# Optimization experiments

Hardware: AMD Instinct MI355X
Metric: run time of the kernel (lower is better)

Reference implementation:

```python
import jax, jax.numpy as jnp
import numpy as np

NUM_GROUPS = 32
EPS = 1e-6


def setup_inputs() -> dict:
    key = jax.random.key(0)
    ks = jax.random.split(key, 4)
    B, C, H, W = 16, 512, 32, 32
    x = jax.random.normal(ks[0], (B, C, H, W), dtype=jnp.float32)
    norm_w = jnp.ones((C,), dtype=jnp.float32)
    norm_b = jnp.zeros((C,), dtype=jnp.float32)
    qkv_w = jax.random.normal(ks[1], (3 * C, C), dtype=jnp.float32) * (1.0 / np.sqrt(C))
    qkv_b = jnp.zeros((3 * C,), dtype=jnp.float32)
    proj_w = jax.random.normal(ks[2], (C, C), dtype=jnp.float32) * (1.0 / np.sqrt(C))
    proj_b = jnp.zeros((C,), dtype=jnp.float32)
    return {"x": x, "norm_w": norm_w, "norm_b": norm_b, "qkv_w": qkv_w,
            "qkv_b": qkv_b, "proj_w": proj_w, "proj_b": proj_b}


def _group_norm(x, w, b):
    B, C, H, W = x.shape
    g = NUM_GROUPS
    xg = x.reshape(B, g, C // g, H * W)
    mu = xg.mean(axis=(2, 3), keepdims=True)
    var = xg.var(axis=(2, 3), keepdims=True)
    xn = (xg - mu) * jax.lax.rsqrt(var + EPS)
    xn = xn.reshape(B, C, H, W)
    return xn * w[None, :, None, None] + b[None, :, None, None]


def reference(x, norm_w, norm_b, qkv_w, qkv_b, proj_w, proj_b):
    B, C, H, W = x.shape
    h = _group_norm(x, norm_w, norm_b)
    # 1x1 conv == channel GEMM
    qkv = jnp.einsum('oc,bchw->bohw', qkv_w, h) + qkv_b[None, :, None, None]
    q, k, v = jnp.split(qkv, 3, axis=1)
    N = H * W
    q = q.reshape(B, C, N)  # (b, c, n)
    k = k.reshape(B, C, N)
    v = v.reshape(B, C, N)
    scale = jnp.asarray(C, x.dtype) ** -0.5
    attn = jnp.einsum('bci,bcj->bij', q, k) * scale  # (b, Nq, Nk)
    attn = jax.nn.softmax(attn, axis=2)
    o = jnp.einsum('bcj,bij->bci', v, attn).reshape(B, C, H, W)
    out = jnp.einsum('oc,bchw->bohw', proj_w, o) + proj_b[None, :, None, None]
    return x + out
```

## Files before the change

kernel.cpp:

```cpp
#include <hip/hip_runtime.h>

typedef unsigned short u16;
typedef __bf16 bf16x8 __attribute__((ext_vector_type(8)));
typedef float f32x4 __attribute__((ext_vector_type(4)));

#define AS1 __attribute__((address_space(1)))
#define AS3 __attribute__((address_space(3)))


__device__ __forceinline__ u16 f2bf(float f) {
  union { float f; unsigned u; } v; v.f = f;
  return (u16)((v.u + 0x7fffu + ((v.u >> 16) & 1u)) >> 16);
}

__device__ __forceinline__ f32x4 mfma16(bf16x8 a, bf16x8 b, f32x4 c) {
  return __builtin_amdgcn_mfma_f32_16x16x32_bf16(a, b, c, 0, 0, 0);
}

__device__ __forceinline__ void stage_tile(const u16* __restrict__ src, size_t ld,
                                           u16* lds, int wv, int lane) {
#pragma unroll
  for (int h2 = 0; h2 < 2; h2++) {
    int rbase = wv * 32 + h2 * 16;
    int row = rbase + (lane >> 2);
    int segd = (lane & 3) ^ ((row >> 1) & 3);
    __builtin_amdgcn_global_load_lds(
        (const AS1 void*)(src + (size_t)row * ld + segd * 8),
        (AS3 void*)(lds + rbase * 32), 16, 0, 0);
  }
}

__device__ __forceinline__ bf16x8 ldsfrag(const u16* lds, int row, int rowq) {
  int q = rowq ^ ((row >> 1) & 3);
  return *(const bf16x8*)(lds + row * 32 + q * 8);
}

template<int NT>
__device__ __forceinline__ void gemm_core(const u16* __restrict__ A, int lda,
                                          const u16* __restrict__ B, int ldb,
                                          u16* lds, f32x4 (&acc)[4][4],
                                          int wave, int lane) {
  u16* sA0 = lds;        u16* sA1 = lds + 4096;
  u16* sB0 = lds + 8192; u16* sB1 = lds + 12288;
  int wm = wave >> 1, wn = wave & 1;
  int col = lane & 15, rq = lane >> 4;
#pragma unroll
  for (int m = 0; m < 4; m++)
#pragma unroll
    for (int n = 0; n < 4; n++) acc[m][n] = (f32x4){0.f, 0.f, 0.f, 0.f};

  stage_tile(A, lda, sA0, wave, lane);
  stage_tile(B, ldb, sB0, wave, lane);
  stage_tile(A + 32, lda, sA1, wave, lane);
  stage_tile(B + 32, ldb, sB1, wave, lane);

  for (int t = 0; t < NT; t++) {
    u16* cA = (t & 1) ? sA1 : sA0;
    u16* cB = (t & 1) ? sB1 : sB0;
    if (t < NT - 1) {
      asm volatile("s_waitcnt vmcnt(4)" ::: "memory");
    } else {
      asm volatile("s_waitcnt vmcnt(0)" ::: "memory");
    }
    __builtin_amdgcn_sched_barrier(0);
    __builtin_amdgcn_s_barrier();
    __builtin_amdgcn_sched_barrier(0);
    bf16x8 af[4], bfr[4];
#pragma unroll
    for (int n = 0; n < 4; n++) bfr[n] = ldsfrag(cB, wn * 64 + n * 16 + col, rq);
#pragma unroll
    for (int m = 0; m < 4; m++) af[m] = ldsfrag(cA, wm * 64 + m * 16 + col, rq);
#pragma unroll
    for (int m = 0; m < 4; m++)
#pragma unroll
      for (int n = 0; n < 4; n++) acc[m][n] = mfma16(af[m], bfr[n], acc[m][n]);
    __builtin_amdgcn_sched_barrier(0);
    __builtin_amdgcn_s_barrier();
    if (t + 2 < NT) {
      stage_tile(A + (size_t)(t + 2) * 32, lda, cA, wave, lane);
      stage_tile(B + (size_t)(t + 2) * 32, ldb, cB, wave, lane);
    }
  }
}

__global__ __launch_bounds__(256) void gn_fused(const float* __restrict__ x,
                                                const float* __restrict__ gw,
                                                const float* __restrict__ gb,
                                                u16* __restrict__ h) {
  __shared__ float buf[16 * 1032];
  __shared__ float ls[4], lss[4];
  int bg = blockIdx.x;
  int b = bg >> 5, g = bg & 31;
  const float4* p = (const float4*)(x + (size_t)bg * 16384);
  float s = 0.f, ss = 0.f;
  for (int i = threadIdx.x; i < 4096; i += 256) {
    float4 v = p[i];
    int c = i >> 8, n = (i & 255) * 4;
    *(float4*)&buf[c * 1032 + n] = v;
    s  += v.x + v.y + v.z + v.w;
    ss += v.x*v.x + v.y*v.y + v.z*v.z + v.w*v.w;
  }
  for (int d = 32; d; d >>= 1) { s += __shfl_down(s, d); ss += __shfl_down(ss, d); }
  int wv = threadIdx.x >> 6;
  if ((threadIdx.x & 63) == 0) { ls[wv] = s; lss[wv] = ss; }
  __syncthreads();
  float m = (ls[0] + ls[1] + ls[2] + ls[3]) * (1.f / 16384.f);
  float var = (lss[0] + lss[1] + lss[2] + lss[3]) * (1.f / 16384.f) - m * m;
  float r = rsqrtf(var + 1e-6f);
  int c0 = g * 16;
  float w[16], bb[16];
#pragma unroll
  for (int c = 0; c < 16; c++) {
    w[c] = gw[c0 + c] * r;
    bb[c] = gb[c0 + c] - m * w[c];
  }
  for (int n = threadIdx.x; n < 1024; n += 256) {
    u16 o[16];
#pragma unroll
    for (int c = 0; c < 16; c++) o[c] = f2bf(buf[c * 1032 + n] * w[c] + bb[c]);
    u16* dst = h + (((size_t)((b << 10) | n)) << 9) + c0;
    *(uint4*)dst = *(uint4*)o;
    *(uint4*)(dst + 8) = *(uint4*)(o + 8);
  }
}

__global__ __launch_bounds__(256) void cast_bf16(const float* __restrict__ src,
                                                 u16* __restrict__ dst, int n) {
  int i = (blockIdx.x * 256 + threadIdx.x) * 4;
  if (i < n) {
    float4 v = *(const float4*)(src + i);
    dst[i] = f2bf(v.x); dst[i+1] = f2bf(v.y); dst[i+2] = f2bf(v.z); dst[i+3] = f2bf(v.w);
  }
}

__global__ __launch_bounds__(256, 4) void gemm_qkv(const u16* __restrict__ A,
                                                   const u16* __restrict__ Bn,
                                                   const float* __restrict__ bias,
                                                   u16* __restrict__ q_nc,
                                                   u16* __restrict__ k_nc,
                                                   u16* __restrict__ v) {
  __shared__ u16 lds[16384];
  int bid = blockIdx.x;
  int xcd = bid & 7, r = bid >> 3;
  int mb = r % 12, nb = xcd * 16 + r / 12;
  int m0 = mb * 128, n0 = nb * 128;
  int t = threadIdx.x, wave = t >> 6, lane = t & 63;
  int wm = wave >> 1, wn = wave & 1;
  int col = lane & 15, rq = lane >> 4;
  f32x4 acc[4][4];
  gemm_core<16>(A + (size_t)m0 * 512, 512, Bn + (size_t)n0 * 512, 512,
                lds, acc, wave, lane);
  if (mb < 8) {
    u16* dst = (mb < 4) ? q_nc : k_nc;
#pragma unroll
    for (int i = 0; i < 4; i++)
#pragma unroll
      for (int j = 0; j < 4; j++) {
        int o = m0 + wm * 64 + i * 16 + rq * 4;
        int bn = n0 + wn * 64 + j * 16 + col;
        u16 tmp[4];
#pragma unroll
        for (int rr = 0; rr < 4; rr++) tmp[rr] = f2bf(acc[i][j][rr] + bias[o + rr]);
        *(uint2*)(dst + (size_t)bn * 512 + (o & 511)) = *(uint2*)tmp;
      }
  } else {
#pragma unroll
    for (int i = 0; i < 4; i++)
#pragma unroll
      for (int j = 0; j < 4; j++)
#pragma unroll
        for (int rr = 0; rr < 4; rr++) {
          int o = m0 + wm * 64 + i * 16 + rq * 4 + rr;
          int bn = n0 + wn * 64 + j * 16 + col;
          v[(size_t)(o & 511) * 16384 + bn] = f2bf(acc[i][j][rr] + bias[o]);
        }
  }
}

__global__ __launch_bounds__(256, 4) void gemm_s(const u16* __restrict__ q_nc,
                                                 const u16* __restrict__ k_nc,
                                                 u16* __restrict__ E,
                                                 float* __restrict__ part) {
  __shared__ u16 lds[16384];
  int bid = blockIdx.x;
  int xcd = bid & 7, r = bid >> 3;
  int b = xcd * 2 + (r & 1);
  int tile = r >> 1;
  int m0 = (tile >> 3) * 128, n0 = (tile & 7) * 128;
  int t = threadIdx.x, wave = t >> 6, lane = t & 63;
  int wm = wave >> 1, wn = wave & 1;
  int col = lane & 15, rq = lane >> 4;
  f32x4 acc[4][4];
  gemm_core<16>(q_nc + ((size_t)(b * 1024 + m0)) * 512, 512,
                k_nc + ((size_t)(b * 1024 + n0)) * 512, 512,
                lds, acc, wave, lane);
  u16* Eb = E + ((size_t)b << 20);
  float* pb = part + ((size_t)b << 14);
  int idx = (n0 >> 6) + wn;
  const float scale = 0.04419417382415922f;
#pragma unroll
  for (int i = 0; i < 4; i++)
#pragma unroll
    for (int rr = 0; rr < 4; rr++) {
      float e[4], rs = 0.f;
#pragma unroll
      for (int j = 0; j < 4; j++) { e[j] = __expf(acc[i][j][rr] * scale); rs += e[j]; }
      rs += __shfl_xor(rs, 1); rs += __shfl_xor(rs, 2);
      rs += __shfl_xor(rs, 4); rs += __shfl_xor(rs, 8);
      int row = m0 + wm * 64 + i * 16 + rq * 4 + rr;
      if (col == 0) pb[row * 16 + idx] = rs;
#pragma unroll
      for (int j = 0; j < 4; j++) {
        int jj = n0 + wn * 64 + j * 16 + col;
        Eb[(size_t)row * 1024 + jj] = f2bf(e[j]);
      }
    }
}

__global__ __launch_bounds__(256) void row_inv2(const float* __restrict__ part,
                                                float* __restrict__ inv) {
  int row = blockIdx.x * 256 + threadIdx.x;
  const float4* p = (const float4*)(part + (size_t)row * 16);
  float4 a = p[0], b = p[1], c = p[2], d = p[3];
  float s = a.x+a.y+a.z+a.w + b.x+b.y+b.z+b.w + c.x+c.y+c.z+c.w + d.x+d.y+d.z+d.w;
  inv[row] = 1.f / s;
}

__global__ __launch_bounds__(256, 4) void gemm_pv(const u16* __restrict__ E,
                                                  const u16* __restrict__ v,
                                                  const float* __restrict__ inv,
                                                  u16* __restrict__ o_nc) {
  __shared__ u16 lds[16384];
  int bid = blockIdx.x;
  int xcd = bid & 7, r = bid >> 3;
  int b = xcd * 2 + (r & 1);
  int tile = r >> 1;
  int m0 = (tile >> 2) * 128, n0 = (tile & 3) * 128;
  int t = threadIdx.x, wave = t >> 6, lane = t & 63;
  int wm = wave >> 1, wn = wave & 1;
  int col = lane & 15, rq = lane >> 4;
  f32x4 acc[4][4];
  gemm_core<32>(E + ((size_t)b << 20) + (size_t)m0 * 1024, 1024,
                v + (size_t)n0 * 16384 + ((size_t)b << 10), 16384,
                lds, acc, wave, lane);
#pragma unroll
  for (int i = 0; i < 4; i++)
#pragma unroll
    for (int rr = 0; rr < 4; rr++) {
      int ii = m0 + wm * 64 + i * 16 + rq * 4 + rr;
      float sc = inv[(b << 10) + ii];
#pragma unroll
      for (int j = 0; j < 4; j++) {
        int cc = n0 + wn * 64 + j * 16 + col;
        o_nc[(((size_t)(b * 1024 + ii)) << 9) + cc] = f2bf(acc[i][j][rr] * sc);
      }
    }
}

__global__ __launch_bounds__(256, 4) void gemm_proj(const u16* __restrict__ A,
                                                    const u16* __restrict__ Bn,
                                                    const float* __restrict__ bias,
                                                    const float* __restrict__ xres,
                                                    float* __restrict__ outp) {
  __shared__ u16 lds[16384];
  int bid = blockIdx.x;
  int xcd = bid & 7, r = bid >> 3;
  int mb = r & 3, nb = xcd * 16 + (r >> 2);
  int m0 = mb * 128, n0 = nb * 128;
  int t = threadIdx.x, wave = t >> 6, lane = t & 63;
  int wm = wave >> 1, wn = wave & 1;
  int col = lane & 15, rq = lane >> 4;
  f32x4 acc[4][4];
  gemm_core<16>(A + (size_t)m0 * 512, 512, Bn + (size_t)n0 * 512, 512,
                lds, acc, wave, lane);
#pragma unroll
  for (int i = 0; i < 4; i++)
#pragma unroll
    for (int j = 0; j < 4; j++)
#pragma unroll
      for (int rr = 0; rr < 4; rr++) {
        int co = m0 + wm * 64 + i * 16 + rq * 4 + rr;
        int bn = n0 + wn * 64 + j * 16 + col;
        int bb = bn >> 10, n = bn & 1023;
        size_t oi = (((size_t)(bb * 512 + co)) << 10) + n;
        outp[oi] = acc[i][j][rr] + bias[co] + xres[oi];
      }
}

extern "C" void kernel_launch(void* const* d_in, const int* in_sizes, int n_in,
                              void* d_out, int out_size, void* d_ws, size_t ws_size,
                              hipStream_t stream) {
  const float* x      = (const float*)d_in[0];
  const float* norm_w = (const float*)d_in[1];
  const float* norm_b = (const float*)d_in[2];
  const float* qkv_w  = (const float*)d_in[3];
  const float* qkv_b  = (const float*)d_in[4];
  const float* proj_w = (const float*)d_in[5];
  const float* proj_b = (const float*)d_in[6];
  float* out = (float*)d_out;

  char* ws = (char*)d_ws;
  size_t off = 0;
  auto alloc = [&](size_t bytes) {
    void* p = ws + off;
    off += (bytes + 255) & ~(size_t)255;
    return p;
  };
  float* part = (float*)alloc((size_t)16384 * 16 * 4);
  float* inv  = (float*)alloc(16384 * 4);
  u16* wq   = (u16*)alloc((size_t)1536 * 512 * 2);
  u16* wp   = (u16*)alloc((size_t)512 * 512 * 2);
  u16* h    = (u16*)alloc((size_t)16384 * 512 * 2);
  u16* q_nc = (u16*)alloc((size_t)16384 * 512 * 2);
  u16* k_nc = (u16*)alloc((size_t)16384 * 512 * 2);
  u16* v    = (u16*)alloc((size_t)512 * 16384 * 2);
  u16* E    = (u16*)alloc((size_t)16 * 1024 * 1024 * 2);
  u16* o_nc = h;
  (void)in_sizes; (void)n_in; (void)out_size; (void)ws_size;

  gn_fused<<<512, 256, 0, stream>>>(x, norm_w, norm_b, h);
  cast_bf16<<<(1536 * 512) / 1024, 256, 0, stream>>>(qkv_w, wq, 1536 * 512);
  cast_bf16<<<(512 * 512) / 1024, 256, 0, stream>>>(proj_w, wp, 512 * 512);
  gemm_qkv<<<1536, 256, 0, stream>>>(wq, h, qkv_b, q_nc, k_nc, v);
  gemm_s<<<1024, 256, 0, stream>>>(q_nc, k_nc, E, part);
  row_inv2<<<64, 256, 0, stream>>>(part, inv);
  gemm_pv<<<512, 256, 0, stream>>>(E, v, inv, o_nc);
  gemm_proj<<<512, 256, 0, stream>>>(wp, o_nc, proj_b, x, out);
}
```

Before: 141.0 us.

## Triple-buffer GEMM LDS pipeline and merge weight cast kernels

The shared GEMM core moves from double to triple buffering. It prefetches three K-tiles ahead, uses graded vmcnt waits and rotates the buffer pointers each iteration. The goal is to hide more global-load latency behind the MFMA work. The cost is 48KB of LDS per block instead of 32KB, and the launch-bounds occupancy hint of 4 is dropped, so fewer blocks may fit per CU. The two weight-cast launches are also merged into one kernel to save a launch.

```diff
diff --git a/kernel.cpp b/kernel.cpp
--- a/kernel.cpp
+++ b/kernel.cpp
@@ -40,8 +40,8 @@
                                           const u16* __restrict__ B, int ldb,
                                           u16* lds, f32x4 (&acc)[4][4],
                                           int wave, int lane) {
-  u16* sA0 = lds;        u16* sA1 = lds + 4096;
-  u16* sB0 = lds + 8192; u16* sB1 = lds + 12288;
+  u16* a0 = lds;         u16* a1 = lds + 4096;  u16* a2 = lds + 8192;
+  u16* b0 = lds + 12288; u16* b1 = lds + 16384; u16* b2 = lds + 20480;
   int wm = wave >> 1, wn = wave & 1;
   int col = lane & 15, rq = lane >> 4;
 #pragma unroll
@@ -49,15 +49,18 @@
 #pragma unroll
     for (int n = 0; n < 4; n++) acc[m][n] = (f32x4){0.f, 0.f, 0.f, 0.f};
 
-  stage_tile(A, lda, sA0, wave, lane);
-  stage_tile(B, ldb, sB0, wave, lane);
-  stage_tile(A + 32, lda, sA1, wave, lane);
-  stage_tile(B + 32, ldb, sB1, wave, lane);
+  stage_tile(A, lda, a0, wave, lane);
+  stage_tile(B, ldb, b0, wave, lane);
+  stage_tile(A + 32, lda, a1, wave, lane);
+  stage_tile(B + 32, ldb, b1, wave, lane);
+  stage_tile(A + 64, lda, a2, wave, lane);
+  stage_tile(B + 64, ldb, b2, wave, lane);
 
   for (int t = 0; t < NT; t++) {
-    u16* cA = (t & 1) ? sA1 : sA0;
-    u16* cB = (t & 1) ? sB1 : sB0;
-    if (t < NT - 1) {
+    int rem = NT - 1 - t;
+    if (rem >= 2) {
+      asm volatile("s_waitcnt vmcnt(8)" ::: "memory");
+    } else if (rem == 1) {
       asm volatile("s_waitcnt vmcnt(4)" ::: "memory");
     } else {
       asm volatile("s_waitcnt vmcnt(0)" ::: "memory");
@@ -67,19 +70,21 @@
     __builtin_amdgcn_sched_barrier(0);
     bf16x8 af[4], bfr[4];
 #pragma unroll
-    for (int n = 0; n < 4; n++) bfr[n] = ldsfrag(cB, wn * 64 + n * 16 + col, rq);
-#pragma unroll
-    for (int m = 0; m < 4; m++) af[m] = ldsfrag(cA, wm * 64 + m * 16 + col, rq);
+    for (int n = 0; n < 4; n++) bfr[n] = ldsfrag(b0, wn * 64 + n * 16 + col, rq);
+#pragma unroll
+    for (int m = 0; m < 4; m++) af[m] = ldsfrag(a0, wm * 64 + m * 16 + col, rq);
 #pragma unroll
     for (int m = 0; m < 4; m++)
 #pragma unroll
       for (int n = 0; n < 4; n++) acc[m][n] = mfma16(af[m], bfr[n], acc[m][n]);
     __builtin_amdgcn_sched_barrier(0);
     __builtin_amdgcn_s_barrier();
-    if (t + 2 < NT) {
-      stage_tile(A + (size_t)(t + 2) * 32, lda, cA, wave, lane);
-      stage_tile(B + (size_t)(t + 2) * 32, ldb, cB, wave, lane);
+    if (t + 3 < NT) {
+      stage_tile(A + (size_t)(t + 3) * 32, lda, a0, wave, lane);
+      stage_tile(B + (size_t)(t + 3) * 32, ldb, b0, wave, lane);
     }
+    u16* ta = a0; a0 = a1; a1 = a2; a2 = ta;
+    u16* tb = b0; b0 = b1; b1 = b2; b2 = tb;
   }
 }
 
@@ -124,22 +129,27 @@
   }
 }
 
-__global__ __launch_bounds__(256) void cast_bf16(const float* __restrict__ src,
-                                                 u16* __restrict__ dst, int n) {
-  int i = (blockIdx.x * 256 + threadIdx.x) * 4;
-  if (i < n) {
-    float4 v = *(const float4*)(src + i);
-    dst[i] = f2bf(v.x); dst[i+1] = f2bf(v.y); dst[i+2] = f2bf(v.z); dst[i+3] = f2bf(v.w);
-  }
-}
-
-__global__ __launch_bounds__(256, 4) void gemm_qkv(const u16* __restrict__ A,
-                                                   const u16* __restrict__ Bn,
-                                                   const float* __restrict__ bias,
-                                                   u16* __restrict__ q_nc,
-                                                   u16* __restrict__ k_nc,
-                                                   u16* __restrict__ v) {
-  __shared__ u16 lds[16384];
+__global__ __launch_bounds__(256) void cast_w(const float* __restrict__ qkv_w,
+                                              float* const ,
+                                              const float* __restrict__ proj_w,
+                                              u16* __restrict__ wq,
+                                              u16* __restrict__ wp) {
+  int bid = blockIdx.x;
+  const float* src = (bid < 768) ? qkv_w : proj_w;
+  u16* dst = (bid < 768) ? wq : wp;
+  int base = (bid < 768) ? bid * 1024 : (bid - 768) * 1024;
+  int i = base + threadIdx.x * 4;
+  float4 v = *(const float4*)(src + i);
+  dst[i] = f2bf(v.x); dst[i+1] = f2bf(v.y); dst[i+2] = f2bf(v.z); dst[i+3] = f2bf(v.w);
+}
+
+__global__ __launch_bounds__(256) void gemm_qkv(const u16* __restrict__ A,
+                                                const u16* __restrict__ Bn,
+                                                const float* __restrict__ bias,
+                                                u16* __restrict__ q_nc,
+                                                u16* __restrict__ k_nc,
+                                                u16* __restrict__ v) {
+  __shared__ u16 lds[24576];
   int bid = blockIdx.x;
   int xcd = bid & 7, r = bid >> 3;
   int mb = r % 12, nb = xcd * 16 + r / 12;
@@ -177,11 +187,11 @@
   }
 }
 
-__global__ __launch_bounds__(256, 4) void gemm_s(const u16* __restrict__ q_nc,
-                                                 const u16* __restrict__ k_nc,
-                                                 u16* __restrict__ E,
-                                                 float* __restrict__ part) {
-  __shared__ u16 lds[16384];
+__global__ __launch_bounds__(256) void gemm_s(const u16* __restrict__ q_nc,
+                                              const u16* __restrict__ k_nc,
+                                              u16* __restrict__ E,
+                                              float* __restrict__ part) {
+  __shared__ u16 lds[24576];
   int bid = blockIdx.x;
   int xcd = bid & 7, r = bid >> 3;
   int b = xcd * 2 + (r & 1);
@@ -226,11 +236,11 @@
   inv[row] = 1.f / s;
 }
 
-__global__ __launch_bounds__(256, 4) void gemm_pv(const u16* __restrict__ E,
-                                                  const u16* __restrict__ v,
-                                                  const float* __restrict__ inv,
-                                                  u16* __restrict__ o_nc) {
-  __shared__ u16 lds[16384];
+__global__ __launch_bounds__(256) void gemm_pv(const u16* __restrict__ E,
+                                               const u16* __restrict__ v,
+                                               const float* __restrict__ inv,
+                                               u16* __restrict__ o_nc) {
+  __shared__ u16 lds[24576];
   int bid = blockIdx.x;
   int xcd = bid & 7, r = bid >> 3;
   int b = xcd * 2 + (r & 1);
@@ -257,12 +267,12 @@
     }
 }
 
-__global__ __launch_bounds__(256, 4) void gemm_proj(const u16* __restrict__ A,
-                                                    const u16* __restrict__ Bn,
-                                                    const float* __restrict__ bias,
-                                                    const float* __restrict__ xres,
-                                                    float* __restrict__ outp) {
-  __shared__ u16 lds[16384];
+__global__ __launch_bounds__(256) void gemm_proj(const u16* __restrict__ A,
+                                                 const u16* __restrict__ Bn,
+                                                 const float* __restrict__ bias,
+                                                 const float* __restrict__ xres,
+                                                 float* __restrict__ outp) {
+  __shared__ u16 lds[24576];
   int bid = blockIdx.x;
   int xcd = bid & 7, r = bid >> 3;
   int mb = r & 3, nb = xcd * 16 + (r >> 2);
@@ -319,8 +329,7 @@
   (void)in_sizes; (void)n_in; (void)out_size; (void)ws_size;
 
   gn_fused<<<512, 256, 0, stream>>>(x, norm_w, norm_b, h);
-  cast_bf16<<<(1536 * 512) / 1024, 256, 0, stream>>>(qkv_w, wq, 1536 * 512);
-  cast_bf16<<<(512 * 512) / 1024, 256, 0, stream>>>(proj_w, wp, 512 * 512);
+  cast_w<<<1024, 256, 0, stream>>>(qkv_w, nullptr, proj_w, wq, wp);
   gemm_qkv<<<1536, 256, 0, stream>>>(wq, h, qkv_b, q_nc, k_nc, v);
   gemm_s<<<1024, 256, 0, stream>>>(q_nc, k_nc, E, part);
   row_inv2<<<64, 256, 0, stream>>>(part, inv);
```

Result: slower. 145.1 us (+2.9%).

## Use 256x256 8-wave GEMM tiles with phased pipeline for QKV and scores

Applied to the files above, without the earlier changes.

Adds a new GEMM core that gives each 512-thread block a 256x256 output tile and a BK=64 double-buffered LDS pipeline. Each K-step is split into four phases, and each phase interleaves the global-to-LDS stage of the next tile with MFMA work under s_setprio. The QKV projection and the QK^T score GEMM now use this core to raise operand reuse and cut global/LDS traffic per FLOP, at the cost of 128KB LDS per block and one block per CU. The two weight-cast launches are merged into one, and the launch-bounds occupancy hints on the PV and projection GEMMs are dropped.

```diff
diff --git a/kernel.cpp b/kernel.cpp
--- a/kernel.cpp
+++ b/kernel.cpp
@@ -36,10 +36,10 @@
 }
 
 template<int NT>
-__device__ __forceinline__ void gemm_core(const u16* __restrict__ A, int lda,
-                                          const u16* __restrict__ B, int ldb,
-                                          u16* lds, f32x4 (&acc)[4][4],
-                                          int wave, int lane) {
+__device__ __forceinline__ void gemm_core2(const u16* __restrict__ A, int lda,
+                                           const u16* __restrict__ B, int ldb,
+                                           u16* lds, f32x4 (&acc)[4][4],
+                                           int wave, int lane) {
   u16* sA0 = lds;        u16* sA1 = lds + 4096;
   u16* sB0 = lds + 8192; u16* sB1 = lds + 12288;
   int wm = wave >> 1, wn = wave & 1;
@@ -80,6 +80,114 @@
       stage_tile(A + (size_t)(t + 2) * 32, lda, cA, wave, lane);
       stage_tile(B + (size_t)(t + 2) * 32, ldb, cB, wave, lane);
     }
+  }
+}
+
+__device__ __forceinline__ void stage_half(const u16* __restrict__ src, size_t ld,
+                                           u16* ldsbase, int wave, int lane) {
+#pragma unroll
+  for (int r = 0; r < 2; r++) {
+    int rb = (r * 8 + wave) * 8;
+    int row = rb + (lane >> 3);
+    int seg = (lane & 7) ^ (row & 7);
+    __builtin_amdgcn_global_load_lds(
+        (const AS1 void*)(src + (size_t)row * ld + seg * 8),
+        (AS3 void*)(ldsbase + rb * 64), 16, 0, 0);
+  }
+}
+
+template<int P>
+__device__ __forceinline__ void phase_read(const u16* cA, const u16* cB,
+                                           bf16x8 (&af)[2][2], bf16x8 (&bfr)[4][2],
+                                           int wm, int wn, int col, int rq) {
+  if constexpr (P == 0) {
+#pragma unroll
+    for (int nf = 0; nf < 4; nf++)
+#pragma unroll
+      for (int kk = 0; kk < 2; kk++) {
+        int row = wn * 64 + nf * 16 + col;
+        bfr[nf][kk] = *(const bf16x8*)(cB + row * 64 + (((kk << 2) + rq) ^ (row & 7)) * 8);
+      }
+  }
+#pragma unroll
+  for (int i = 0; i < 2; i++)
+#pragma unroll
+    for (int kk = 0; kk < 2; kk++) {
+      int row = wm * 128 + (P * 2 + i) * 16 + col;
+      af[i][kk] = *(const bf16x8*)(cA + row * 64 + (((kk << 2) + rq) ^ (row & 7)) * 8);
+    }
+}
+
+template<int P>
+__device__ __forceinline__ void phase_fma(const bf16x8 (&af)[2][2],
+                                          const bf16x8 (&bfr)[4][2],
+                                          f32x4 (&acc)[8][4]) {
+#pragma unroll
+  for (int i = 0; i < 2; i++)
+#pragma unroll
+    for (int kk = 0; kk < 2; kk++)
+#pragma unroll
+      for (int nf = 0; nf < 4; nf++)
+        acc[P * 2 + i][nf] = mfma16(af[i][kk], bfr[nf][kk], acc[P * 2 + i][nf]);
+}
+
+#define RUN_PHASE(P, STAGE_CODE, WAIT_CODE)                                  \
+  {                                                                          \
+    bf16x8 af[2][2];                                                         \
+    phase_read<P>(cA, cB, af, bfr, wm, wn, col, rq);                         \
+    STAGE_CODE;                                                              \
+    WAIT_CODE;                                                               \
+    __builtin_amdgcn_sched_barrier(0);                                       \
+    __builtin_amdgcn_s_barrier();                                            \
+    __builtin_amdgcn_sched_barrier(0);                                       \
+    __builtin_amdgcn_s_setprio(1);                                           \
+    phase_fma<P>(af, bfr, acc);                                              \
+    __builtin_amdgcn_s_setprio(0);                                           \
+    __builtin_amdgcn_sched_barrier(0);                                       \
+    __builtin_amdgcn_s_barrier();                                            \
+    __builtin_amdgcn_sched_barrier(0);                                       \
+  }
+
+template<int NT>
+__device__ __forceinline__ void gemm8_core(const u16* __restrict__ A, int lda,
+                                           const u16* __restrict__ B, int ldb,
+                                           u16* lds, f32x4 (&acc)[8][4],
+                                           int wave, int lane) {
+  u16* Abuf[2] = {lds, lds + 16384};
+  u16* Bbuf[2] = {lds + 32768, lds + 49152};
+  int wm = wave >> 2, wn = wave & 3;
+  int col = lane & 15, rq = lane >> 4;
+#pragma unroll
+  for (int m = 0; m < 8; m++)
+#pragma unroll
+    for (int n = 0; n < 4; n++) acc[m][n] = (f32x4){0.f, 0.f, 0.f, 0.f};
+
+  stage_half(A, lda, Abuf[0], wave, lane);
+  stage_half(A + 128 * (size_t)lda, lda, Abuf[0] + 8192, wave, lane);
+  stage_half(B, ldb, Bbuf[0], wave, lane);
+  stage_half(B + 128 * (size_t)ldb, ldb, Bbuf[0] + 8192, wave, lane);
+  stage_half(B + 64, ldb, Bbuf[1], wave, lane);
+  stage_half(B + 64 + 128 * (size_t)ldb, ldb, Bbuf[1] + 8192, wave, lane);
+  asm volatile("s_waitcnt vmcnt(4)" ::: "memory");
+  __builtin_amdgcn_sched_barrier(0);
+  __builtin_amdgcn_s_barrier();
+  __builtin_amdgcn_sched_barrier(0);
+
+  for (int kt = 0; kt < NT; kt++) {
+    const u16* cA = Abuf[kt & 1];
+    const u16* cB = Bbuf[kt & 1];
+    u16* nA = Abuf[(kt + 1) & 1];
+    u16* nB = Bbuf[kt & 1];
+    const u16* Asrc = A + (size_t)(kt + 1) * 64;
+    const u16* Bsrc = B + (size_t)(kt + 2) * 64;
+    bool pa = (kt + 1 < NT), pb = (kt + 2 < NT);
+    bf16x8 bfr[4][2];
+    RUN_PHASE(0, if (pa) stage_half(Asrc, lda, nA, wave, lane), );
+    RUN_PHASE(1, if (pa) stage_half(Asrc + 128 * (size_t)lda, lda, nA + 8192, wave, lane), );
+    RUN_PHASE(2, if (pb) stage_half(Bsrc, ldb, nB, wave, lane), );
+    RUN_PHASE(3, if (pb) stage_half(Bsrc + 128 * (size_t)ldb, ldb, nB + 8192, wave, lane),
+              if (pb) { asm volatile("s_waitcnt vmcnt(4)" ::: "memory"); }
+              else    { asm volatile("s_waitcnt vmcnt(0)" ::: "memory"); });
   }
 }
 
@@ -124,74 +232,78 @@
   }
 }
 
-__global__ __launch_bounds__(256) void cast_bf16(const float* __restrict__ src,
-                                                 u16* __restrict__ dst, int n) {
-  int i = (blockIdx.x * 256 + threadIdx.x) * 4;
-  if (i < n) {
-    float4 v = *(const float4*)(src + i);
-    dst[i] = f2bf(v.x); dst[i+1] = f2bf(v.y); dst[i+2] = f2bf(v.z); dst[i+3] = f2bf(v.w);
-  }
-}
-
-__global__ __launch_bounds__(256, 4) void gemm_qkv(const u16* __restrict__ A,
-                                                   const u16* __restrict__ Bn,
-                                                   const float* __restrict__ bias,
-                                                   u16* __restrict__ q_nc,
-                                                   u16* __restrict__ k_nc,
-                                                   u16* __restrict__ v) {
-  __shared__ u16 lds[16384];
+__global__ __launch_bounds__(256) void cast_w(const float* __restrict__ qkv_w,
+                                              const float* __restrict__ proj_w,
+                                              u16* __restrict__ wq,
+                                              u16* __restrict__ wp) {
+  int bid = blockIdx.x;
+  const float* src = (bid < 768) ? qkv_w : proj_w;
+  u16* dst = (bid < 768) ? wq : wp;
+  int base = (bid < 768) ? bid * 1024 : (bid - 768) * 1024;
+  int i = base + threadIdx.x * 4;
+  float4 v = *(const float4*)(src + i);
+  dst[i] = f2bf(v.x); dst[i+1] = f2bf(v.y); dst[i+2] = f2bf(v.z); dst[i+3] = f2bf(v.w);
+}
+
+__global__ __launch_bounds__(512, 1) void gemm8_qkv(const u16* __restrict__ A,
+                                                    const u16* __restrict__ Bn,
+                                                    const float* __restrict__ bias,
+                                                    u16* __restrict__ q_nc,
+                                                    u16* __restrict__ k_nc,
+                                                    u16* __restrict__ v) {
+  __shared__ u16 lds[65536];
   int bid = blockIdx.x;
   int xcd = bid & 7, r = bid >> 3;
-  int mb = r % 12, nb = xcd * 16 + r / 12;
-  int m0 = mb * 128, n0 = nb * 128;
+  int mb = r % 6, nb = xcd * 8 + r / 6;
+  int m0 = mb * 256, n0 = nb * 256;
   int t = threadIdx.x, wave = t >> 6, lane = t & 63;
-  int wm = wave >> 1, wn = wave & 1;
-  int col = lane & 15, rq = lane >> 4;
-  f32x4 acc[4][4];
-  gemm_core<16>(A + (size_t)m0 * 512, 512, Bn + (size_t)n0 * 512, 512,
+  int wm = wave >> 2, wn = wave & 3;
+  int col = lane & 15, rq = lane >> 4;
+  f32x4 acc[8][4];
+  gemm8_core<8>(A + (size_t)m0 * 512, 512, Bn + (size_t)n0 * 512, 512,
                 lds, acc, wave, lane);
-  if (mb < 8) {
-    u16* dst = (mb < 4) ? q_nc : k_nc;
-#pragma unroll
-    for (int i = 0; i < 4; i++)
-#pragma unroll
-      for (int j = 0; j < 4; j++) {
-        int o = m0 + wm * 64 + i * 16 + rq * 4;
-        int bn = n0 + wn * 64 + j * 16 + col;
+  if (mb < 4) {
+    u16* dst = (mb < 2) ? q_nc : k_nc;
+#pragma unroll
+    for (int mf = 0; mf < 8; mf++)
+#pragma unroll
+      for (int nf = 0; nf < 4; nf++) {
+        int o = m0 + wm * 128 + mf * 16 + rq * 4;
+        int bn = n0 + wn * 64 + nf * 16 + col;
         u16 tmp[4];
 #pragma unroll
-        for (int rr = 0; rr < 4; rr++) tmp[rr] = f2bf(acc[i][j][rr] + bias[o + rr]);
+        for (int rr = 0; rr < 4; rr++) tmp[rr] = f2bf(acc[mf][nf][rr] + bias[o + rr]);
         *(uint2*)(dst + (size_t)bn * 512 + (o & 511)) = *(uint2*)tmp;
       }
   } else {
 #pragma unroll
-    for (int i = 0; i < 4; i++)
-#pragma unroll
-      for (int j = 0; j < 4; j++)
+    for (int mf = 0; mf < 8; mf++)
+#pragma unroll
+      for (int nf = 0; nf < 4; nf++)
 #pragma unroll
         for (int rr = 0; rr < 4; rr++) {
-          int o = m0 + wm * 64 + i * 16 + rq * 4 + rr;
-          int bn = n0 + wn * 64 + j * 16 + col;
-          v[(size_t)(o & 511) * 16384 + bn] = f2bf(acc[i][j][rr] + bias[o]);
+          int o = m0 + wm * 128 + mf * 16 + rq * 4 + rr;
+          int bn = n0 + wn * 64 + nf * 16 + col;
+          v[(size_t)(o & 511) * 16384 + bn] = f2bf(acc[mf][nf][rr] + bias[o]);
         }
   }
 }
 
-__global__ __launch_bounds__(256, 4) void gemm_s(const u16* __restrict__ q_nc,
-                                                 const u16* __restrict__ k_nc,
-                                                 u16* __restrict__ E,
-                                                 float* __restrict__ part) {
-  __shared__ u16 lds[16384];
+__global__ __launch_bounds__(512, 1) void gemm8_s(const u16* __restrict__ q_nc,
+                                                  const u16* __restrict__ k_nc,
+                                                  u16* __restrict__ E,
+                                                  float* __restrict__ part) {
+  __shared__ u16 lds[65536];
   int bid = blockIdx.x;
   int xcd = bid & 7, r = bid >> 3;
   int b = xcd * 2 + (r & 1);
   int tile = r >> 1;
-  int m0 = (tile >> 3) * 128, n0 = (tile & 7) * 128;
+  int m0 = (tile >> 2) * 256, n0 = (tile & 3) * 256;
   int t = threadIdx.x, wave = t >> 6, lane = t & 63;
-  int wm = wave >> 1, wn = wave & 1;
-  int col = lane & 15, rq = lane >> 4;
-  f32x4 acc[4][4];
-  gemm_core<16>(q_nc + ((size_t)(b * 1024 + m0)) * 512, 512,
+  int wm = wave >> 2, wn = wave & 3;
+  int col = lane & 15, rq = lane >> 4;
+  f32x4 acc[8][4];
+  gemm8_core<8>(q_nc + ((size_t)(b * 1024 + m0)) * 512, 512,
                 k_nc + ((size_t)(b * 1024 + n0)) * 512, 512,
                 lds, acc, wave, lane);
   u16* Eb = E + ((size_t)b << 20);
@@ -199,20 +311,20 @@
   int idx = (n0 >> 6) + wn;
   const float scale = 0.04419417382415922f;
 #pragma unroll
-  for (int i = 0; i < 4; i++)
+  for (int mf = 0; mf < 8; mf++)
 #pragma unroll
     for (int rr = 0; rr < 4; rr++) {
       float e[4], rs = 0.f;
 #pragma unroll
-      for (int j = 0; j < 4; j++) { e[j] = __expf(acc[i][j][rr] * scale); rs += e[j]; }
+      for (int nf = 0; nf < 4; nf++) { e[nf] = __expf(acc[mf][nf][rr] * scale); rs += e[nf]; }
       rs += __shfl_xor(rs, 1); rs += __shfl_xor(rs, 2);
       rs += __shfl_xor(rs, 4); rs += __shfl_xor(rs, 8);
-      int row = m0 + wm * 64 + i * 16 + rq * 4 + rr;
+      int row = m0 + wm * 128 + mf * 16 + rq * 4 + rr;
       if (col == 0) pb[row * 16 + idx] = rs;
 #pragma unroll
-      for (int j = 0; j < 4; j++) {
-        int jj = n0 + wn * 64 + j * 16 + col;
-        Eb[(size_t)row * 1024 + jj] = f2bf(e[j]);
+      for (int nf = 0; nf < 4; nf++) {
+        int jj = n0 + wn * 64 + nf * 16 + col;
+        Eb[(size_t)row * 1024 + jj] = f2bf(e[nf]);
       }
     }
 }
@@ -226,10 +338,10 @@
   inv[row] = 1.f / s;
 }
 
-__global__ __launch_bounds__(256, 4) void gemm_pv(const u16* __restrict__ E,
-                                                  const u16* __restrict__ v,
-                                                  const float* __restrict__ inv,
-                                                  u16* __restrict__ o_nc) {
+__global__ __launch_bounds__(256) void gemm_pv(const u16* __restrict__ E,
+                                               const u16* __restrict__ v,
+                                               const float* __restrict__ inv,
+                                               u16* __restrict__ o_nc) {
   __shared__ u16 lds[16384];
   int bid = blockIdx.x;
   int xcd = bid & 7, r = bid >> 3;
@@ -240,9 +352,9 @@
   int wm = wave >> 1, wn = wave & 1;
   int col = lane & 15, rq = lane >> 4;
   f32x4 acc[4][4];
-  gemm_core<32>(E + ((size_t)b << 20) + (size_t)m0 * 1024, 1024,
-                v + (size_t)n0 * 16384 + ((size_t)b << 10), 16384,
-                lds, acc, wave, lane);
+  gemm_core2<32>(E + ((size_t)b << 20) + (size_t)m0 * 1024, 1024,
+                 v + (size_t)n0 * 16384 + ((size_t)b << 10), 16384,
+                 lds, acc, wave, lane);
 #pragma unroll
   for (int i = 0; i < 4; i++)
 #pragma unroll
@@ -257,11 +369,11 @@
     }
 }
 
-__global__ __launch_bounds__(256, 4) void gemm_proj(const u16* __restrict__ A,
-                                                    const u16* __restrict__ Bn,
-                                                    const float* __restrict__ bias,
-                                                    const float* __restrict__ xres,
-                                                    float* __restrict__ outp) {
+__global__ __launch_bounds__(256) void gemm_proj(const u16* __restrict__ A,
+                                                 const u16* __restrict__ Bn,
+                                                 const float* __restrict__ bias,
+                                                 const float* __restrict__ xres,
+                                                 float* __restrict__ outp) {
   __shared__ u16 lds[16384];
   int bid = blockIdx.x;
   int xcd = bid & 7, r = bid >> 3;
@@ -271,8 +383,8 @@
   int wm = wave >> 1, wn = wave & 1;
   int col = lane & 15, rq = lane >> 4;
   f32x4 acc[4][4];
-  gemm_core<16>(A + (size_t)m0 * 512, 512, Bn + (size_t)n0 * 512, 512,
-                lds, acc, wave, lane);
+  gemm_core2<16>(A + (size_t)m0 * 512, 512, Bn + (size_t)n0 * 512, 512,
+                 lds, acc, wave, lane);
 #pragma unroll
   for (int i = 0; i < 4; i++)
 #pragma unroll
@@ -319,10 +431,9 @@
   (void)in_sizes; (void)n_in; (void)out_size; (void)ws_size;
 
   gn_fused<<<512, 256, 0, stream>>>(x, norm_w, norm_b, h);
-  cast_bf16<<<(1536 * 512) / 1024, 256, 0, stream>>>(qkv_w, wq, 1536 * 512);
-  cast_bf16<<<(512 * 512) / 1024, 256, 0, stream>>>(proj_w, wp, 512 * 512);
-  gemm_qkv<<<1536, 256, 0, stream>>>(wq, h, qkv_b, q_nc, k_nc, v);
-  gemm_s<<<1024, 256, 0, stream>>>(q_nc, k_nc, E, part);
+  cast_w<<<1024, 256, 0, stream>>>(qkv_w, proj_w, wq, wp);
+  gemm8_qkv<<<384, 512, 0, stream>>>(wq, h, qkv_b, q_nc, k_nc, v);
+  gemm8_s<<<256, 512, 0, stream>>>(q_nc, k_nc, E, part);
   row_inv2<<<64, 256, 0, stream>>>(part, inv);
   gemm_pv<<<512, 256, 0, stream>>>(E, v, inv, o_nc);
   gemm_proj<<<512, 256, 0, stream>>>(wp, o_nc, proj_b, x, out);
```

New measurement: 138.6 us. Within noise of the previous version (-1.7%).

## Stage GEMM epilogues through LDS for coalesced 16-byte stores; merge weight casts

Applied to the files above, without the earlier changes.

The qkv, S and PV GEMM epilogues now write results into a padded LDS tile (row stride 132) and then flush it with 16-byte row-contiguous global stores. Before, they did scattered 2-byte or 8-byte stores, including strided transposed writes for V. The two weight-cast launches are merged into one kernel to save a launch. The LDS buffer grows slightly and extra barriers are added, which may affect occupancy and adds an LDS round trip.

```diff
diff --git a/kernel.cpp b/kernel.cpp
--- a/kernel.cpp
+++ b/kernel.cpp
@@ -36,10 +36,10 @@
 }
 
 template<int NT>
-__device__ __forceinline__ void gemm_core(const u16* __restrict__ A, int lda,
-                                          const u16* __restrict__ B, int ldb,
-                                          u16* lds, f32x4 (&acc)[4][4],
-                                          int wave, int lane) {
+__device__ __forceinline__ void gemm_core2(const u16* __restrict__ A, int lda,
+                                           const u16* __restrict__ B, int ldb,
+                                           u16* lds, f32x4 (&acc)[4][4],
+                                           int wave, int lane) {
   u16* sA0 = lds;        u16* sA1 = lds + 4096;
   u16* sB0 = lds + 8192; u16* sB1 = lds + 12288;
   int wm = wave >> 1, wn = wave & 1;
@@ -80,6 +80,16 @@
       stage_tile(A + (size_t)(t + 2) * 32, lda, cA, wave, lane);
       stage_tile(B + (size_t)(t + 2) * 32, ldb, cB, wave, lane);
     }
+  }
+}
+
+__device__ __forceinline__ void epi_flush(const u16* lds, u16* gdst, size_t stride, int t) {
+#pragma unroll
+  for (int pass = 0; pass < 8; pass++) {
+    int row = pass * 16 + (t >> 4);
+    int ch = (t & 15) * 8;
+    uint4 w = *(const uint4*)(lds + row * 132 + ch);
+    *(uint4*)(gdst + (size_t)row * stride + ch) = w;
   }
 }
 
@@ -124,13 +134,17 @@
   }
 }
 
-__global__ __launch_bounds__(256) void cast_bf16(const float* __restrict__ src,
-                                                 u16* __restrict__ dst, int n) {
-  int i = (blockIdx.x * 256 + threadIdx.x) * 4;
-  if (i < n) {
-    float4 v = *(const float4*)(src + i);
-    dst[i] = f2bf(v.x); dst[i+1] = f2bf(v.y); dst[i+2] = f2bf(v.z); dst[i+3] = f2bf(v.w);
-  }
+__global__ __launch_bounds__(256) void cast_w(const float* __restrict__ qkv_w,
+                                              const float* __restrict__ proj_w,
+                                              u16* __restrict__ wq,
+                                              u16* __restrict__ wp) {
+  int bid = blockIdx.x;
+  const float* src = (bid < 768) ? qkv_w : proj_w;
+  u16* dst = (bid < 768) ? wq : wp;
+  int base = (bid < 768) ? bid * 1024 : (bid - 768) * 1024;
+  int i = base + threadIdx.x * 4;
+  float4 v = *(const float4*)(src + i);
+  dst[i] = f2bf(v.x); dst[i+1] = f2bf(v.y); dst[i+2] = f2bf(v.z); dst[i+3] = f2bf(v.w);
 }
 
 __global__ __launch_bounds__(256, 4) void gemm_qkv(const u16* __restrict__ A,
@@ -139,7 +153,7 @@
                                                    u16* __restrict__ q_nc,
                                                    u16* __restrict__ k_nc,
                                                    u16* __restrict__ v) {
-  __shared__ u16 lds[16384];
+  __shared__ u16 lds[16896];
   int bid = blockIdx.x;
   int xcd = bid & 7, r = bid >> 3;
   int mb = r % 12, nb = xcd * 16 + r / 12;
@@ -148,21 +162,25 @@
   int wm = wave >> 1, wn = wave & 1;
   int col = lane & 15, rq = lane >> 4;
   f32x4 acc[4][4];
-  gemm_core<16>(A + (size_t)m0 * 512, 512, Bn + (size_t)n0 * 512, 512,
-                lds, acc, wave, lane);
+  gemm_core2<16>(A + (size_t)m0 * 512, 512, Bn + (size_t)n0 * 512, 512,
+                 lds, acc, wave, lane);
+  __syncthreads();
   if (mb < 8) {
-    u16* dst = (mb < 4) ? q_nc : k_nc;
 #pragma unroll
     for (int i = 0; i < 4; i++)
 #pragma unroll
       for (int j = 0; j < 4; j++) {
         int o = m0 + wm * 64 + i * 16 + rq * 4;
-        int bn = n0 + wn * 64 + j * 16 + col;
         u16 tmp[4];
 #pragma unroll
         for (int rr = 0; rr < 4; rr++) tmp[rr] = f2bf(acc[i][j][rr] + bias[o + rr]);
-        *(uint2*)(dst + (size_t)bn * 512 + (o & 511)) = *(uint2*)tmp;
+        int bnl = wn * 64 + j * 16 + col;
+        int chl = wm * 64 + i * 16 + rq * 4;
+        *(uint2*)(lds + bnl * 132 + chl) = *(uint2*)tmp;
       }
+    __syncthreads();
+    u16* dst = ((mb < 4) ? q_nc : k_nc) + (size_t)n0 * 512 + (m0 & 511);
+    epi_flush(lds, dst, 512, t);
   } else {
 #pragma unroll
     for (int i = 0; i < 4; i++)
@@ -171,9 +189,13 @@
 #pragma unroll
         for (int rr = 0; rr < 4; rr++) {
           int o = m0 + wm * 64 + i * 16 + rq * 4 + rr;
-          int bn = n0 + wn * 64 + j * 16 + col;
-          v[(size_t)(o & 511) * 16384 + bn] = f2bf(acc[i][j][rr] + bias[o]);
+          int chl = wm * 64 + i * 16 + rq * 4 + rr;
+          int bnl = wn * 64 + j * 16 + col;
+          lds[chl * 132 + bnl] = f2bf(acc[i][j][rr] + bias[o]);
         }
+    __syncthreads();
+    u16* dst = v + (size_t)(m0 - 1024) * 16384 + n0;
+    epi_flush(lds, dst, 16384, t);
   }
 }
 
@@ -181,7 +203,7 @@
                                                  const u16* __restrict__ k_nc,
                                                  u16* __restrict__ E,
                                                  float* __restrict__ part) {
-  __shared__ u16 lds[16384];
+  __shared__ u16 lds[16896];
   int bid = blockIdx.x;
   int xcd = bid & 7, r = bid >> 3;
   int b = xcd * 2 + (r & 1);
@@ -191,13 +213,13 @@
   int wm = wave >> 1, wn = wave & 1;
   int col = lane & 15, rq = lane >> 4;
   f32x4 acc[4][4];
-  gemm_core<16>(q_nc + ((size_t)(b * 1024 + m0)) * 512, 512,
-                k_nc + ((size_t)(b * 1024 + n0)) * 512, 512,
-                lds, acc, wave, lane);
-  u16* Eb = E + ((size_t)b << 20);
+  gemm_core2<16>(q_nc + ((size_t)(b * 1024 + m0)) * 512, 512,
+                 k_nc + ((size_t)(b * 1024 + n0)) * 512, 512,
+                 lds, acc, wave, lane);
   float* pb = part + ((size_t)b << 14);
   int idx = (n0 >> 6) + wn;
   const float scale = 0.04419417382415922f;
+  __syncthreads();
 #pragma unroll
   for (int i = 0; i < 4; i++)
 #pragma unroll
@@ -207,14 +229,14 @@
       for (int j = 0; j < 4; j++) { e[j] = __expf(acc[i][j][rr] * scale); rs += e[j]; }
       rs += __shfl_xor(rs, 1); rs += __shfl_xor(rs, 2);
       rs += __shfl_xor(rs, 4); rs += __shfl_xor(rs, 8);
-      int row = m0 + wm * 64 + i * 16 + rq * 4 + rr;
-      if (col == 0) pb[row * 16 + idx] = rs;
-#pragma unroll
-      for (int j = 0; j < 4; j++) {
-        int jj = n0 + wn * 64 + j * 16 + col;
-        Eb[(size_t)row * 1024 + jj] = f2bf(e[j]);
-      }
+      int iil = wm * 64 + i * 16 + rq * 4 + rr;
+      if (col == 0) pb[(m0 + iil) * 16 + idx] = rs;
+#pragma unroll
+      for (int j = 0; j < 4; j++)
+        lds[iil * 132 + wn * 64 + j * 16 + col] = f2bf(e[j]);
     }
+  __syncthreads();
+  epi_flush(lds, E + ((size_t)b << 20) + (size_t)m0 * 1024 + n0, 1024, t);
 }
 
 __global__ __launch_bounds__(256) void row_inv2(const float* __restrict__ part,
@@ -230,7 +252,7 @@
                                                   const u16* __restrict__ v,
                                                   const float* __restrict__ inv,
                                                   u16* __restrict__ o_nc) {
-  __shared__ u16 lds[16384];
+  __shared__ u16 lds[16896];
   int bid = blockIdx.x;
   int xcd = bid & 7, r = bid >> 3;
   int b = xcd * 2 + (r & 1);
@@ -240,21 +262,22 @@
   int wm = wave >> 1, wn = wave & 1;
   int col = lane & 15, rq = lane >> 4;
   f32x4 acc[4][4];
-  gemm_core<32>(E + ((size_t)b << 20) + (size_t)m0 * 1024, 1024,
-                v + (size_t)n0 * 16384 + ((size_t)b << 10), 16384,
-                lds, acc, wave, lane);
+  gemm_core2<32>(E + ((size_t)b << 20) + (size_t)m0 * 1024, 1024,
+                 v + (size_t)n0 * 16384 + ((size_t)b << 10), 16384,
+                 lds, acc, wave, lane);
+  __syncthreads();
 #pragma unroll
   for (int i = 0; i < 4; i++)
 #pragma unroll
     for (int rr = 0; rr < 4; rr++) {
-      int ii = m0 + wm * 64 + i * 16 + rq * 4 + rr;
-      float sc = inv[(b << 10) + ii];
-#pragma unroll
-      for (int j = 0; j < 4; j++) {
-        int cc = n0 + wn * 64 + j * 16 + col;
-        o_nc[(((size_t)(b * 1024 + ii)) << 9) + cc] = f2bf(acc[i][j][rr] * sc);
-      }
+      int iil = wm * 64 + i * 16 + rq * 4 + rr;
+      float sc = inv[(b << 10) + m0 + iil];
+#pragma unroll
+      for (int j = 0; j < 4; j++)
+        lds[iil * 132 + wn * 64 + j * 16 + col] = f2bf(acc[i][j][rr] * sc);
     }
+  __syncthreads();
+  epi_flush(lds, o_nc + ((size_t)(b * 1024 + m0)) * 512 + n0, 512, t);
 }
 
 __global__ __launch_bounds__(256, 4) void gemm_proj(const u16* __restrict__ A,
@@ -271,8 +294,8 @@
   int wm = wave >> 1, wn = wave & 1;
   int col = lane & 15, rq = lane >> 4;
   f32x4 acc[4][4];
-  gemm_core<16>(A + (size_t)m0 * 512, 512, Bn + (size_t)n0 * 512, 512,
-                lds, acc, wave, lane);
+  gemm_core2<16>(A + (size_t)m0 * 512, 512, Bn + (size_t)n0 * 512, 512,
+                 lds, acc, wave, lane);
 #pragma unroll
   for (int i = 0; i < 4; i++)
 #pragma unroll
@@ -319,8 +342,7 @@
   (void)in_sizes; (void)n_in; (void)out_size; (void)ws_size;
 
   gn_fused<<<512, 256, 0, stream>>>(x, norm_w, norm_b, h);
-  cast_bf16<<<(1536 * 512) / 1024, 256, 0, stream>>>(qkv_w, wq, 1536 * 512);
-  cast_bf16<<<(512 * 512) / 1024, 256, 0, stream>>>(proj_w, wp, 512 * 512);
+  cast_w<<<1024, 256, 0, stream>>>(qkv_w, proj_w, wq, wp);
   gemm_qkv<<<1536, 256, 0, stream>>>(wq, h, qkv_b, q_nc, k_nc, v);
   gemm_s<<<1024, 256, 0, stream>>>(q_nc, k_nc, E, part);
   row_inv2<<<64, 256, 0, stream>>>(part, inv);
```

Result: no change. 139.7 us (-1.0%).
